# Optimization experiments

Measured on AMD Instinct MI355X. Metric: run time of the kernel, lower is better.

Reference implementation:

```python
import jax, jax.numpy as jnp
import numpy as np

DIM = 2048
N_HEADS = 16
HEAD_DIM = DIM // N_HEADS  # 128
KV_RANK = 512
MAX_SEQ = 2048
EPS = 1e-6


def _precompute_freqs(dim, end, theta=10000.0):
    freqs = 1.0 / theta ** (np.arange(0, dim, 2)[: dim // 2].astype(np.float32) / dim)
    t = np.arange(end, dtype=np.float32)
    ang = np.outer(t, freqs)  # [end, dim//2]
    return jnp.asarray(np.cos(ang)), jnp.asarray(np.sin(ang))


def setup_inputs() -> dict:
    key = jax.random.key(0)
    ks = jax.random.split(key, 6)
    s = 0.02
    x = jax.random.normal(ks[0], (1, 2048, DIM), dtype=jnp.float32)
    wq = jax.random.normal(ks[1], (N_HEADS * HEAD_DIM, DIM), dtype=jnp.float32) * s
    w_kv_down = jax.random.normal(ks[2], (KV_RANK, DIM), dtype=jnp.float32) * s
    w_kv_up = jax.random.normal(ks[3], (2 * N_HEADS * HEAD_DIM, KV_RANK), dtype=jnp.float32) * s
    wo = jax.random.normal(ks[4], (DIM, N_HEADS * HEAD_DIM), dtype=jnp.float32) * s
    q_norm_w = jnp.ones((HEAD_DIM,), dtype=jnp.float32)
    k_norm_w = jnp.ones((HEAD_DIM,), dtype=jnp.float32)
    freqs_cos, freqs_sin = _precompute_freqs(HEAD_DIM, MAX_SEQ)
    return {"x": x, "wq": wq, "w_kv_down": w_kv_down, "w_kv_up": w_kv_up,
            "wo": wo, "q_norm_w": q_norm_w, "k_norm_w": k_norm_w,
            "freqs_cos": freqs_cos, "freqs_sin": freqs_sin}


def _rmsnorm(x, w):
    var = jnp.mean(x * x, axis=-1, keepdims=True)
    return x * jax.lax.rsqrt(var + EPS) * w


def _rope(x, cos, sin):
    # x: [B,T,H,D] -> pairs [B,T,H,D/2,2]; cos/sin: [T,D/2] broadcast over heads
    xr = x.reshape(*x.shape[:-1], -1, 2)
    re, im = xr[..., 0], xr[..., 1]
    c = cos[None, :, None, :]
    s = sin[None, :, None, :]
    out = jnp.stack([re * c - im * s, re * s + im * c], axis=-1)
    return out.reshape(x.shape)


def reference(x, wq, w_kv_down, w_kv_up, wo, q_norm_w, k_norm_w, freqs_cos, freqs_sin):
    B, T, C = x.shape
    H, D = N_HEADS, HEAD_DIM
    xq = jnp.einsum('btc,ec->bte', x, wq).reshape(B, T, H, D)
    latent = jnp.einsum('btc,rc->btr', x, w_kv_down)            # [B,T,R]
    kv = jnp.einsum('btr,er->bte', latent, w_kv_up).reshape(B, T, 2, H, D)
    xk, xv = kv[:, :, 0], kv[:, :, 1]
    xq = _rmsnorm(xq, q_norm_w)
    xk = _rmsnorm(xk, k_norm_w)
    cos, sin = freqs_cos[:T], freqs_sin[:T]
    xq = _rope(xq, cos, sin)
    xk = _rope(xk, cos, sin)
    scale = 1.0 / jnp.sqrt(jnp.asarray(D, dtype=x.dtype))
    scores = jnp.einsum('bthd,bshd->bhts', xq, xk) * scale       # [B,H,T,T]
    causal = jnp.tril(jnp.ones((T, T), dtype=bool))
    scores = jnp.where(causal, scores, jnp.finfo(scores.dtype).min)
    attn = jax.nn.softmax(scores, axis=-1)
    out = jnp.einsum('bhts,bshd->bthd', attn, xv).reshape(B, T, C)
    return jnp.einsum('bte,ce->btc', out, wo)
```

## Files before the change

kernel.cpp:

```cpp
#include <hip/hip_runtime.h>

#define T_SEQ 2048
#define DIM   2048
#define NH    16
#define HD    128
#define KVR   512

typedef unsigned short ushort_t;
typedef __attribute__((ext_vector_type(8))) short   short8;
typedef __attribute__((ext_vector_type(8))) __bf16  bf16x8;
typedef __attribute__((ext_vector_type(4))) float   f32x4;
typedef __attribute__((ext_vector_type(4))) unsigned int u32x4;

union V8 { short8 s; bf16x8 b; u32x4 u; };

__device__ inline float b2f(ushort_t u) {
    union { unsigned u; float f; } x; x.u = ((unsigned)u) << 16; return x.f;
}
__device__ inline ushort_t f2b(float f) {
    union { float f; unsigned u; } x; x.f = f;
    unsigned r = x.u + 0x7FFFu + ((x.u >> 16) & 1u);
    return (ushort_t)(r >> 16);
}

__device__ __forceinline__ void gld16(char* lds, const ushort_t* g) {
    __builtin_amdgcn_global_load_lds(
        (const __attribute__((address_space(1))) unsigned int*)g,
        (__attribute__((address_space(3))) unsigned int*)lds,
        16, 0, 0);
}

__global__ __launch_bounds__(256) void cvtk(
    const float* __restrict__ a0, const float* __restrict__ a1,
    const float* __restrict__ a2, const float* __restrict__ a3,
    const float* __restrict__ a4,
    ushort_t* __restrict__ b0, ushort_t* __restrict__ b1,
    ushort_t* __restrict__ b2, ushort_t* __restrict__ b3,
    ushort_t* __restrict__ b4)
{
    const int N0 = 524288, N1 = 1048576, N2 = 1179648, N3 = 1441792, N4 = 1966080;
    for (int c = blockIdx.x * blockDim.x + threadIdx.x; c < N4; c += gridDim.x * blockDim.x) {
        const float* s; ushort_t* d; int off;
        if      (c < N0) { s = a0; d = b0; off = c; }
        else if (c < N1) { s = a1; d = b1; off = c - N0; }
        else if (c < N2) { s = a2; d = b2; off = c - N1; }
        else if (c < N3) { s = a3; d = b3; off = c - N2; }
        else             { s = a4; d = b4; off = c - N3; }
        f32x4 lo = *(const f32x4*)(s + (size_t)off * 8);
        f32x4 hi = *(const f32x4*)(s + (size_t)off * 8 + 4);
        V8 v;
        #pragma unroll
        for (int e = 0; e < 4; ++e) { v.b[e] = (__bf16)lo[e]; v.b[e + 4] = (__bf16)hi[e]; }
        *(u32x4*)(d + (size_t)off * 8) = v.u;
    }
}

template <bool OUT_F32>
__global__ __launch_bounds__(256, 2) void gemm_nt(
    const ushort_t* __restrict__ A, const ushort_t* __restrict__ B,
    void* __restrict__ Cv, int M, int K,
    const ushort_t* __restrict__ B2, void* __restrict__ C2, int Nsplit, int N2)
{
    __shared__ __align__(16) char sA[2][16384];
    __shared__ __align__(16) char sB[2][16384];

    const int tid  = threadIdx.x;
    const int wave = tid >> 6;
    const int lane = tid & 63;
    const int l15  = lane & 15;
    const int l4   = lane >> 4;

    const int gridX = gridDim.x;
    int idlin = blockIdx.y * gridX + blockIdx.x;
    const int cpx = (gridX * gridDim.y) >> 3;
    idlin = (idlin & 7) * cpx + (idlin >> 3);
    const int bm = (idlin % gridX) * 128;
    const int bn = (idlin / gridX) * 128;

    const ushort_t* Bp = B;
    void* Cp = Cv; int ldC = Nsplit; int bnl = bn;
    if (B2 != nullptr && bn >= Nsplit) { Bp = B2; Cp = C2; ldC = N2; bnl = bn - Nsplit; }

    const int wm = (wave >> 1) * 64;
    const int wn = (wave & 1) * 64;

    const int lp   = lane ^ ((lane >> 3) & 7);
    const int prow = lp >> 3;
    const int psub = lp & 7;
    const ushort_t* aSrc[4];
    const ushort_t* bSrc[4];
    #pragma unroll
    for (int i = 0; i < 4; ++i) {
        int r = wave * 32 + i * 8 + prow;
        aSrc[i] = A  + (size_t)(bm  + r) * K + psub * 8;
        bSrc[i] = Bp + (size_t)(bnl + r) * K + psub * 8;
    }
    const int ldsOff = wave * 4096;

    f32x4 acc[4][4] = {};
    const int nk = K >> 6;

    #pragma unroll
    for (int i = 0; i < 4; ++i) {
        gld16(&sA[0][ldsOff + i * 1024], aSrc[i]);
        gld16(&sB[0][ldsOff + i * 1024], bSrc[i]);
    }

    int cur = 0;
    for (int k = 0; k < nk; ++k) {
        __syncthreads();
        if (k + 1 < nk) {
            const int ko = (k + 1) * 64;
            #pragma unroll
            for (int i = 0; i < 4; ++i) {
                gld16(&sA[cur ^ 1][ldsOff + i * 1024], aSrc[i] + ko);
                gld16(&sB[cur ^ 1][ldsOff + i * 1024], bSrc[i] + ko);
            }
        }
        #pragma unroll
        for (int kk = 0; kk < 2; ++kk) {
            V8 a[4], b[4];
            #pragma unroll
            for (int i2 = 0; i2 < 4; ++i2) {
                int row = wm + i2 * 16 + l15;
                a[i2].u = *(const u32x4*)(sA[cur] + ((row * 128 + kk * 64 + l4 * 16) ^ ((row & 7) << 4)));
                int col = wn + i2 * 16 + l15;
                b[i2].u = *(const u32x4*)(sB[cur] + ((col * 128 + kk * 64 + l4 * 16) ^ ((col & 7) << 4)));
            }
            #pragma unroll
            for (int i2 = 0; i2 < 4; ++i2)
                #pragma unroll
                for (int j = 0; j < 4; ++j)
                    acc[i2][j] = __builtin_amdgcn_mfma_f32_16x16x32_bf16(a[i2].b, b[j].b, acc[i2][j], 0, 0, 0);
        }
        cur ^= 1;
    }

    #pragma unroll
    for (int i = 0; i < 4; ++i)
        #pragma unroll
        for (int j = 0; j < 4; ++j)
            #pragma unroll
            for (int r = 0; r < 4; ++r) {
                int rowg = bm + wm + i * 16 + l4 * 4 + r;
                int colg = bnl + wn + j * 16 + l15;
                if constexpr (OUT_F32)
                    ((float*)Cp)[(size_t)rowg * ldC + colg] = acc[i][j][r];
                else
                    ((ushort_t*)Cp)[(size_t)rowg * ldC + colg] = f2b(acc[i][j][r]);
            }
}

__global__ __launch_bounds__(256) void norm_rope2(
    ushort_t* __restrict__ Qb, ushort_t* __restrict__ KVb,
    const float* __restrict__ QW, const float* __restrict__ KW,
    const float* __restrict__ FC, const float* __restrict__ FS)
{
    const int b    = blockIdx.x;
    const bool isK = b >= 2048;
    const int t    = b & 2047;
    const int tid  = threadIdx.x;
    const int h    = tid >> 4;
    const int sub  = tid & 15;

    ushort_t* X      = isK ? KVb : Qb;
    const float* W   = isK ? KW : QW;
    const int stride = isK ? 4096 : 2048;

    ushort_t* p = X + (size_t)t * stride + h * HD + sub * 8;
    V8 v; v.u = *(const u32x4*)p;
    float f[8];
    #pragma unroll
    for (int e = 0; e < 8; ++e) f[e] = b2f((ushort_t)v.s[e]);

    float ss = 0.f;
    #pragma unroll
    for (int e = 0; e < 8; ++e) ss += f[e] * f[e];
    ss += __shfl_xor(ss, 1);
    ss += __shfl_xor(ss, 2);
    ss += __shfl_xor(ss, 4);
    ss += __shfl_xor(ss, 8);
    float inv = rsqrtf(ss * (1.0f / 128.0f) + 1e-6f);

    float outv[8];
    #pragma unroll
    for (int k = 0; k < 4; ++k) {
        float c  = FC[(size_t)t * 64 + sub * 4 + k];
        float s  = FS[(size_t)t * 64 + sub * 4 + k];
        float w0 = W[sub * 8 + 2 * k];
        float w1 = W[sub * 8 + 2 * k + 1];
        float re = f[2 * k] * inv * w0;
        float im = f[2 * k + 1] * inv * w1;
        outv[2 * k]     = re * c - im * s;
        outv[2 * k + 1] = re * s + im * c;
    }
    V8 o;
    #pragma unroll
    for (int e = 0; e < 8; ++e) o.s[e] = (short)f2b(outv[e]);
    *(u32x4*)p = o.u;
}

#define STAGE_LOAD(kv0) do { \
  _Pragma("unroll") for (int rr = 0; rr < 4; ++rr) \
    kreg[rr] = *(const u32x4*)(KV + (size_t)((kv0) + krow[rr]) * (2 * DIM) + h * HD + kc8 * 8); \
  _Pragma("unroll") for (int rr = 0; rr < 2; ++rr) \
    _Pragma("unroll") for (int e = 0; e < 8; ++e) \
      vreg[rr][e] = *(const unsigned*)(KV + (size_t)((kv0) + vkvb[rr] * 8 + e) * (2 * DIM) + DIM + h * HD + vd); \
} while (0)

#define STAGE_WRITE(sKb, sVb) do { \
  _Pragma("unroll") for (int rr = 0; rr < 4; ++rr) \
    *(u32x4*)((sKb) + ((krow[rr] * 256 + kc8 * 16) ^ ((krow[rr] & 7) << 4))) = kreg[rr]; \
  _Pragma("unroll") for (int rr = 0; rr < 2; ++rr) { \
    V8 lo, hi; \
    _Pragma("unroll") for (int e = 0; e < 8; ++e) { \
      lo.s[e] = (short)(vreg[rr][e] & 0xFFFFu); hi.s[e] = (short)(vreg[rr][e] >> 16); } \
    *(u32x4*)((sVb) + ((vd * 128 + vkvb[rr] * 16) ^ ((vd & 7) << 4)))             = lo.u; \
    *(u32x4*)((sVb) + (((vd + 1) * 128 + vkvb[rr] * 16) ^ (((vd + 1) & 7) << 4))) = hi.u; \
  } \
} while (0)

__global__ __launch_bounds__(512) void attn_kernel(
    const ushort_t* __restrict__ Q,
    const ushort_t* __restrict__ KV,
    ushort_t* __restrict__ O)
{
    __shared__ __align__(16) char sAll[131072];

    const int id    = blockIdx.x;
    const int xcd   = id & 7;
    const int slot  = id >> 3;
    const int h     = xcd * 2 + (slot >> 4);
    const int pairb = slot & 15;

    const int tid   = threadIdx.x;
    const int gid   = tid >> 8;
    const int wtid  = tid & 255;
    const int wave4 = wtid >> 6;
    const int lane  = tid & 63;
    const int Qq    = lane & 15;
    const int G     = lane >> 4;

    char* gbase = sAll + gid * 65536;

    const int krow[4] = { (0*256 + wtid) >> 4, (1*256 + wtid) >> 4,
                          (2*256 + wtid) >> 4, (3*256 + wtid) >> 4 };
    const int kc8 = wtid & 15;
    const int vd  = lane * 2;
    const int vkvb[2] = { wave4, 4 + wave4 };

    const float scale2 = 0.08838834764831845f * 1.4426950408889634f;
    const float THR2   = 11.541560327111707f;

    u32x4 kreg[4];
    unsigned vreg[2][8];

    #pragma unroll
    for (int phase = 0; phase < 2; ++phase) {
        const int jt  = phase ? (31 - pairb) : pairb;
        const int q0w = jt * 64 + wave4 * 16;

        V8 qf[4];
        #pragma unroll
        for (int kk = 0; kk < 4; ++kk)
            qf[kk].u = *(const u32x4*)(Q + (size_t)(q0w + Qq) * DIM + h * HD + kk * 32 + G * 8);

        f32x4 o[8] = {};
        float mrow = -1e30f, lrow = 0.f;

        const int n_g = (jt >= gid) ? ((jt - gid) >> 1) + 1 : 0;
        const int nA  = (jt >> 1) + 1;

        if (n_g > 0) {
            STAGE_LOAD(gid * 64);
            STAGE_WRITE(gbase, gbase + 32768);
        }

        int cur = 0;
        for (int s = 0; s < nA; ++s) {
            __syncthreads();

            const bool pf = (s + 1 < n_g);
            if (pf) STAGE_LOAD((2 * (s + 1) + gid) * 64);

            if (s < n_g) {
                const int tcur = 2 * s + gid;
                const int kv0  = tcur * 64;
                char* sKb = gbase + cur * 16384;
                char* sVb = gbase + 32768 + cur * 16384;

                f32x4 sacc[4] = {};
                __builtin_amdgcn_s_setprio(1);
                #pragma unroll
                for (int kk = 0; kk < 4; ++kk) {
                    #pragma unroll
                    for (int cb = 0; cb < 4; ++cb) {
                        int row = cb * 16 + Qq;
                        V8 kf;
                        kf.u = *(const u32x4*)(sKb + ((row * 256 + kk * 64 + G * 16) ^ ((row & 7) << 4)));
                        sacc[cb] = __builtin_amdgcn_mfma_f32_16x16x32_bf16(kf.b, qf[kk].b, sacc[cb], 0, 0, 0);
                    }
                }
                __builtin_amdgcn_s_setprio(0);

                float p[4][4];
                float tmax = -3e38f;
                const int qg = q0w + Qq;
                #pragma unroll
                for (int cb = 0; cb < 4; ++cb)
                    #pragma unroll
                    for (int r = 0; r < 4; ++r) {
                        float s2 = sacc[cb][r] * scale2;
                        if (tcur == jt) {
                            int kvg = kv0 + cb * 16 + G * 4 + r;
                            if (kvg > qg) s2 = -1e30f;
                        }
                        p[cb][r] = s2;
                        tmax = fmaxf(tmax, s2);
                    }
                tmax = fmaxf(tmax, __shfl_xor(tmax, 16));
                tmax = fmaxf(tmax, __shfl_xor(tmax, 32));

                const bool skip = __all(tmax - mrow <= THR2);
                float corr = 1.0f;
                if (!skip) {
                    const float mnew = fmaxf(mrow, tmax);
                    corr = exp2f(mrow - mnew);
                    mrow = mnew;
                }
                float rs = 0.f;
                #pragma unroll
                for (int cb = 0; cb < 4; ++cb)
                    #pragma unroll
                    for (int r = 0; r < 4; ++r) {
                        float e = exp2f(p[cb][r] - mrow);
                        p[cb][r] = e;
                        rs += e;
                    }
                rs += __shfl_xor(rs, 16);
                rs += __shfl_xor(rs, 32);
                lrow = lrow * corr + rs;

                unsigned pk[4][2];
                #pragma unroll
                for (int cb = 0; cb < 4; ++cb) {
                    pk[cb][0] = (unsigned)f2b(p[cb][0]) | ((unsigned)f2b(p[cb][1]) << 16);
                    pk[cb][1] = (unsigned)f2b(p[cb][2]) | ((unsigned)f2b(p[cb][3]) << 16);
                }

                if (!skip) {
                    float cf[4];
                    #pragma unroll
                    for (int r = 0; r < 4; ++r)
                        cf[r] = __shfl(corr, G * 4 + r);
                    #pragma unroll
                    for (int nb = 0; nb < 8; ++nb)
                        #pragma unroll
                        for (int r = 0; r < 4; ++r)
                            o[nb][r] *= cf[r];
                }

                const int sLo = ((G & 1) * 2) * 16 + Qq;
                const int sHi = sLo + 16;
                const bool hiC = (G >> 1);
                #pragma unroll
                for (int kk2 = 0; kk2 < 2; ++kk2) {
                    const int c0 = kk2 * 2, c1 = c0 + 1;
                    unsigned w0a = __shfl(pk[c0][0], sLo), w0b = __shfl(pk[c1][0], sLo);
                    unsigned w1a = __shfl(pk[c0][1], sLo), w1b = __shfl(pk[c1][1], sLo);
                    unsigned w2a = __shfl(pk[c0][0], sHi), w2b = __shfl(pk[c1][0], sHi);
                    unsigned w3a = __shfl(pk[c0][1], sHi), w3b = __shfl(pk[c1][1], sHi);
                    V8 pa;
                    pa.u[0] = hiC ? w0b : w0a;
                    pa.u[1] = hiC ? w1b : w1a;
                    pa.u[2] = hiC ? w2b : w2a;
                    pa.u[3] = hiC ? w3b : w3a;
                    __builtin_amdgcn_s_setprio(1);
                    #pragma unroll
                    for (int nb = 0; nb < 8; ++nb) {
                        int d = nb * 16 + Qq;
                        V8 vf;
                        vf.u = *(const u32x4*)(sVb + ((d * 128 + kk2 * 64 + G * 16) ^ ((d & 7) << 4)));
                        o[nb] = __builtin_amdgcn_mfma_f32_16x16x32_bf16(pa.b, vf.b, o[nb], 0, 0, 0);
                    }
                    __builtin_amdgcn_s_setprio(0);
                }
            }

            if (pf) STAGE_WRITE(gbase + (cur ^ 1) * 16384, gbase + 32768 + (cur ^ 1) * 16384);
            cur ^= 1;
        }

        __syncthreads();
        float* mrg = (float*)sAll;
        float* mlb = (float*)(sAll + 33792);
        if (gid == 1) {
            #pragma unroll
            for (int nb = 0; nb < 8; ++nb)
                #pragma unroll
                for (int r = 0; r < 4; ++r) {
                    int qloc = wave4 * 16 + G * 4 + r;
                    mrg[qloc * 132 + nb * 16 + Qq] = o[nb][r];
                }
            if (G == 0) {
                int qloc = wave4 * 16 + Qq;
                mlb[qloc]      = mrow;
                mlb[64 + qloc] = lrow;
            }
        }
        __syncthreads();
        if (gid == 0) {
            int qloc0 = wave4 * 16 + Qq;
            float mB = mlb[qloc0], lB = mlb[64 + qloc0];
            float m  = fmaxf(mrow, mB);
            float cA = exp2f(mrow - m), cB = exp2f(mB - m);
            float linv = 1.f / (lrow * cA + lB * cB);
            float cAr[4], cBr[4], lir[4];
            #pragma unroll
            for (int r = 0; r < 4; ++r) {
                cAr[r] = __shfl(cA, G * 4 + r);
                cBr[r] = __shfl(cB, G * 4 + r);
                lir[r] = __shfl(linv, G * 4 + r);
            }
            #pragma unroll
            for (int nb = 0; nb < 8; ++nb)
                #pragma unroll
                for (int r = 0; r < 4; ++r) {
                    int qloc = wave4 * 16 + G * 4 + r;
                    float ob  = mrg[qloc * 132 + nb * 16 + Qq];
                    float val = (o[nb][r] * cAr[r] + ob * cBr[r]) * lir[r];
                    int qgr = jt * 64 + qloc;
                    O[(size_t)qgr * DIM + h * HD + nb * 16 + Qq] = f2b(val);
                }
        }
        __syncthreads();
    }
}

extern "C" void kernel_launch(void* const* d_in, const int* in_sizes, int n_in,
                              void* d_out, int out_size, void* d_ws, size_t ws_size,
                              hipStream_t stream)
{
    const float* x    = (const float*)d_in[0];
    const float* wq   = (const float*)d_in[1];
    const float* wkvd = (const float*)d_in[2];
    const float* wkvu = (const float*)d_in[3];
    const float* wo   = (const float*)d_in[4];
    const float* qnw  = (const float*)d_in[5];
    const float* knw  = (const float*)d_in[6];
    const float* fc   = (const float*)d_in[7];
    const float* fs   = (const float*)d_in[8];
    float* out = (float*)d_out;

    char* ws = (char*)d_ws;
    const size_t MB = 1024 * 1024;
    ushort_t* xb    = (ushort_t*)(ws);
    ushort_t* att   = (ushort_t*)(ws);
    ushort_t* Qb    = (ushort_t*)(ws + 8  * MB);
    ushort_t* wqb   = (ushort_t*)(ws + 16 * MB);
    ushort_t* wkvdb = (ushort_t*)(ws + 24 * MB);
    ushort_t* kvb   = (ushort_t*)(ws + 16 * MB);
    ushort_t* lat   = (ushort_t*)(ws + 32 * MB);
    ushort_t* wkvub = (ushort_t*)(ws + 34 * MB);
    ushort_t* wob   = (ushort_t*)(ws + 38 * MB);

    cvtk<<<dim3(2048), dim3(256), 0, stream>>>(x, wq, wkvd, wkvu, wo,
                                               xb, wqb, wkvdb, wkvub, wob);
    gemm_nt<false><<<dim3(16, 20), dim3(256), 0, stream>>>(xb, wqb, Qb, 2048, 2048,
                                                           wkvdb, lat, 2048, 512);
    gemm_nt<false><<<dim3(16, 32), dim3(256), 0, stream>>>(lat, wkvub, kvb, 2048, 512,
                                                           nullptr, nullptr, 4096, 0);
    norm_rope2<<<dim3(4096), dim3(256), 0, stream>>>(Qb, kvb, qnw, knw, fc, fs);
    attn_kernel<<<dim3(256), dim3(512), 0, stream>>>(Qb, kvb, att);
    gemm_nt<true><<<dim3(16, 16), dim3(256), 0, stream>>>(att, wob, out, 2048, 2048,
                                                          nullptr, nullptr, 2048, 0);
}
```

Measured before the change: 174.3 us.

## Fuse Q RMSNorm and RoPE into projection GEMM epilogue, retile GEMMs

The GEMM is templated on block sizes so the Q/latent projection uses 64x128 tiles, with each block covering one full head. This lets the epilogue compute the per-row RMS sum via shuffles and shared memory and apply norm and RoPE before writing Q. The standalone norm kernel now handles only K, and the output projection moves to 128x64 tiles so more blocks launch. The aim is to drop one read/write pass over Q and fill the GPU better, at the cost of smaller tiles with less data reuse and a heavier epilogue.

```diff
diff --git a/kernel.cpp b/kernel.cpp
--- a/kernel.cpp
+++ b/kernel.cpp
@@ -55,14 +55,22 @@
     }
 }
 
-template <bool OUT_F32>
+template <int BM, int BN, bool OUT_F32, bool NORMQ>
 __global__ __launch_bounds__(256, 2) void gemm_nt(
     const ushort_t* __restrict__ A, const ushort_t* __restrict__ B,
     void* __restrict__ Cv, int M, int K,
-    const ushort_t* __restrict__ B2, void* __restrict__ C2, int Nsplit, int N2)
+    const ushort_t* __restrict__ B2, void* __restrict__ C2, int Nsplit, int N2,
+    const float* __restrict__ NW, const float* __restrict__ FC,
+    const float* __restrict__ FS)
 {
-    __shared__ __align__(16) char sA[2][16384];
-    __shared__ __align__(16) char sB[2][16384];
+    constexpr int GM = BM / 64;
+    constexpr int WN = BN * GM / 4;
+    constexpr int NJ = WN / 16;
+    constexpr int AR = BM / 32;
+    constexpr int BR = BN / 32;
+
+    __shared__ __align__(16) char sA[2][BM * 128];
+    __shared__ __align__(16) char sB[2][BN * 128];
 
     const int tid  = threadIdx.x;
     const int wave = tid >> 6;
@@ -74,37 +82,42 @@
     int idlin = blockIdx.y * gridX + blockIdx.x;
     const int cpx = (gridX * gridDim.y) >> 3;
     idlin = (idlin & 7) * cpx + (idlin >> 3);
-    const int bm = (idlin % gridX) * 128;
-    const int bn = (idlin / gridX) * 128;
+    const int bm = (idlin % gridX) * BM;
+    const int bn = (idlin / gridX) * BN;
 
     const ushort_t* Bp = B;
     void* Cp = Cv; int ldC = Nsplit; int bnl = bn;
-    if (B2 != nullptr && bn >= Nsplit) { Bp = B2; Cp = C2; ldC = N2; bnl = bn - Nsplit; }
-
-    const int wm = (wave >> 1) * 64;
-    const int wn = (wave & 1) * 64;
+    bool second = false;
+    if (B2 != nullptr && bn >= Nsplit) { Bp = B2; Cp = C2; ldC = N2; bnl = bn - Nsplit; second = true; }
+
+    const int wmo = (GM == 2) ? (wave >> 1) * 64 : 0;
+    const int wno = (GM == 2) ? (wave & 1) * WN : wave * WN;
 
     const int lp   = lane ^ ((lane >> 3) & 7);
     const int prow = lp >> 3;
     const int psub = lp & 7;
-    const ushort_t* aSrc[4];
-    const ushort_t* bSrc[4];
-    #pragma unroll
-    for (int i = 0; i < 4; ++i) {
-        int r = wave * 32 + i * 8 + prow;
-        aSrc[i] = A  + (size_t)(bm  + r) * K + psub * 8;
+    const ushort_t* aSrc[AR];
+    const ushort_t* bSrc[BR];
+    #pragma unroll
+    for (int i = 0; i < AR; ++i) {
+        int r = wave * (BM / 4) + i * 8 + prow;
+        aSrc[i] = A + (size_t)(bm + r) * K + psub * 8;
+    }
+    #pragma unroll
+    for (int i = 0; i < BR; ++i) {
+        int r = wave * (BN / 4) + i * 8 + prow;
         bSrc[i] = Bp + (size_t)(bnl + r) * K + psub * 8;
     }
-    const int ldsOff = wave * 4096;
-
-    f32x4 acc[4][4] = {};
+    const int ldsOffA = wave * (BM * 32);
+    const int ldsOffB = wave * (BN * 32);
+
+    f32x4 acc[4][NJ] = {};
     const int nk = K >> 6;
 
     #pragma unroll
-    for (int i = 0; i < 4; ++i) {
-        gld16(&sA[0][ldsOff + i * 1024], aSrc[i]);
-        gld16(&sB[0][ldsOff + i * 1024], bSrc[i]);
-    }
+    for (int i = 0; i < AR; ++i) gld16(&sA[0][ldsOffA + i * 1024], aSrc[i]);
+    #pragma unroll
+    for (int i = 0; i < BR; ++i) gld16(&sB[0][ldsOffB + i * 1024], bSrc[i]);
 
     int cur = 0;
     for (int k = 0; k < nk; ++k) {
@@ -112,38 +125,81 @@
         if (k + 1 < nk) {
             const int ko = (k + 1) * 64;
             #pragma unroll
-            for (int i = 0; i < 4; ++i) {
-                gld16(&sA[cur ^ 1][ldsOff + i * 1024], aSrc[i] + ko);
-                gld16(&sB[cur ^ 1][ldsOff + i * 1024], bSrc[i] + ko);
-            }
+            for (int i = 0; i < AR; ++i) gld16(&sA[cur ^ 1][ldsOffA + i * 1024], aSrc[i] + ko);
+            #pragma unroll
+            for (int i = 0; i < BR; ++i) gld16(&sB[cur ^ 1][ldsOffB + i * 1024], bSrc[i] + ko);
         }
         #pragma unroll
         for (int kk = 0; kk < 2; ++kk) {
-            V8 a[4], b[4];
+            V8 a[4], b[NJ];
             #pragma unroll
             for (int i2 = 0; i2 < 4; ++i2) {
-                int row = wm + i2 * 16 + l15;
+                int row = wmo + i2 * 16 + l15;
                 a[i2].u = *(const u32x4*)(sA[cur] + ((row * 128 + kk * 64 + l4 * 16) ^ ((row & 7) << 4)));
-                int col = wn + i2 * 16 + l15;
-                b[i2].u = *(const u32x4*)(sB[cur] + ((col * 128 + kk * 64 + l4 * 16) ^ ((col & 7) << 4)));
+            }
+            #pragma unroll
+            for (int j = 0; j < NJ; ++j) {
+                int col = wno + j * 16 + l15;
+                b[j].u = *(const u32x4*)(sB[cur] + ((col * 128 + kk * 64 + l4 * 16) ^ ((col & 7) << 4)));
             }
             #pragma unroll
             for (int i2 = 0; i2 < 4; ++i2)
                 #pragma unroll
-                for (int j = 0; j < 4; ++j)
+                for (int j = 0; j < NJ; ++j)
                     acc[i2][j] = __builtin_amdgcn_mfma_f32_16x16x32_bf16(a[i2].b, b[j].b, acc[i2][j], 0, 0, 0);
         }
         cur ^= 1;
     }
 
+    const bool doNorm = NORMQ && !second;
+    if (doNorm) {
+        __syncthreads();
+        float* sums = (float*)sA;
+        #pragma unroll
+        for (int i = 0; i < 4; ++i)
+            #pragma unroll
+            for (int r = 0; r < 4; ++r) {
+                float ss = 0.f;
+                #pragma unroll
+                for (int j = 0; j < NJ; ++j) ss += acc[i][j][r] * acc[i][j][r];
+                ss += __shfl_xor(ss, 1);
+                ss += __shfl_xor(ss, 2);
+                ss += __shfl_xor(ss, 4);
+                ss += __shfl_xor(ss, 8);
+                if (l15 == 0) sums[wave * 64 + i * 16 + l4 * 4 + r] = ss;
+            }
+        __syncthreads();
+        #pragma unroll
+        for (int i = 0; i < 4; ++i)
+            #pragma unroll
+            for (int r = 0; r < 4; ++r) {
+                const int rloc = i * 16 + l4 * 4 + r;
+                const float tot = sums[rloc] + sums[64 + rloc] + sums[128 + rloc] + sums[192 + rloc];
+                const float inv = rsqrtf(tot * (1.0f / 128.0f) + 1e-6f);
+                const int t = bm + rloc;
+                #pragma unroll
+                for (int j = 0; j < NJ; ++j) {
+                    const int col = wno + j * 16 + l15;
+                    float v = acc[i][j][r] * inv * NW[col];
+                    float partner = __shfl_xor(v, 1);
+                    const float c = FC[(size_t)t * 64 + (col >> 1)];
+                    const float s = FS[(size_t)t * 64 + (col >> 1)];
+                    float outv = (l15 & 1) ? (partner * s + v * c)
+                                           : (v * c - partner * s);
+                    ((ushort_t*)Cp)[(size_t)t * ldC + bnl + col] = f2b(outv);
+                }
+            }
+        return;
+    }
+
     #pragma unroll
     for (int i = 0; i < 4; ++i)
         #pragma unroll
-        for (int j = 0; j < 4; ++j)
+        for (int j = 0; j < NJ; ++j)
             #pragma unroll
             for (int r = 0; r < 4; ++r) {
-                int rowg = bm + wm + i * 16 + l4 * 4 + r;
-                int colg = bnl + wn + j * 16 + l15;
+                int rowg = bm + wmo + i * 16 + l4 * 4 + r;
+                int colg = bnl + wno + j * 16 + l15;
                 if constexpr (OUT_F32)
                     ((float*)Cp)[(size_t)rowg * ldC + colg] = acc[i][j][r];
                 else
@@ -151,23 +207,16 @@
             }
 }
 
-__global__ __launch_bounds__(256) void norm_rope2(
-    ushort_t* __restrict__ Qb, ushort_t* __restrict__ KVb,
-    const float* __restrict__ QW, const float* __restrict__ KW,
+__global__ __launch_bounds__(256) void norm_ropeK(
+    ushort_t* __restrict__ KVb, const float* __restrict__ KW,
     const float* __restrict__ FC, const float* __restrict__ FS)
 {
-    const int b    = blockIdx.x;
-    const bool isK = b >= 2048;
-    const int t    = b & 2047;
-    const int tid  = threadIdx.x;
-    const int h    = tid >> 4;
-    const int sub  = tid & 15;
-
-    ushort_t* X      = isK ? KVb : Qb;
-    const float* W   = isK ? KW : QW;
-    const int stride = isK ? 4096 : 2048;
-
-    ushort_t* p = X + (size_t)t * stride + h * HD + sub * 8;
+    const int t   = blockIdx.x;
+    const int tid = threadIdx.x;
+    const int h   = tid >> 4;
+    const int sub = tid & 15;
+
+    ushort_t* p = KVb + (size_t)t * 4096 + h * HD + sub * 8;
     V8 v; v.u = *(const u32x4*)p;
     float f[8];
     #pragma unroll
@@ -187,8 +236,8 @@
     for (int k = 0; k < 4; ++k) {
         float c  = FC[(size_t)t * 64 + sub * 4 + k];
         float s  = FS[(size_t)t * 64 + sub * 4 + k];
-        float w0 = W[sub * 8 + 2 * k];
-        float w1 = W[sub * 8 + 2 * k + 1];
+        float w0 = KW[sub * 8 + 2 * k];
+        float w1 = KW[sub * 8 + 2 * k + 1];
         float re = f[2 * k] * inv * w0;
         float im = f[2 * k + 1] * inv * w1;
         outv[2 * k]     = re * c - im * s;
@@ -466,12 +515,12 @@
 
     cvtk<<<dim3(2048), dim3(256), 0, stream>>>(x, wq, wkvd, wkvu, wo,
                                                xb, wqb, wkvdb, wkvub, wob);
-    gemm_nt<false><<<dim3(16, 20), dim3(256), 0, stream>>>(xb, wqb, Qb, 2048, 2048,
-                                                           wkvdb, lat, 2048, 512);
-    gemm_nt<false><<<dim3(16, 32), dim3(256), 0, stream>>>(lat, wkvub, kvb, 2048, 512,
-                                                           nullptr, nullptr, 4096, 0);
-    norm_rope2<<<dim3(4096), dim3(256), 0, stream>>>(Qb, kvb, qnw, knw, fc, fs);
+    gemm_nt<64, 128, false, true><<<dim3(32, 20), dim3(256), 0, stream>>>(
+        xb, wqb, Qb, 2048, 2048, wkvdb, lat, 2048, 512, qnw, fc, fs);
+    gemm_nt<128, 128, false, false><<<dim3(16, 32), dim3(256), 0, stream>>>(
+        lat, wkvub, kvb, 2048, 512, nullptr, nullptr, 4096, 0, nullptr, nullptr, nullptr);
+    norm_ropeK<<<dim3(2048), dim3(256), 0, stream>>>(kvb, knw, fc, fs);
     attn_kernel<<<dim3(256), dim3(512), 0, stream>>>(Qb, kvb, att);
-    gemm_nt<true><<<dim3(16, 16), dim3(256), 0, stream>>>(att, wob, out, 2048, 2048,
-                                                          nullptr, nullptr, 2048, 0);
-}
+    gemm_nt<128, 64, true, false><<<dim3(16, 32), dim3(256), 0, stream>>>(
+        att, wob, out, 2048, 2048, nullptr, nullptr, 2048, 0, nullptr, nullptr, nullptr);
+}
```

Result: faster. 159.1 us (-8.7%).
